# Performance work log

Hardware: AMD Instinct MI355X
Metric: run time of the kernel (lower is better)

The kernel has to match this reference:

```python
import jax, jax.numpy as jnp
import numpy as np

CORR_WIDTH = 48
H_RADIUS = 3
V_RADIUS = 3


def _unfold_patches(img, vr, hr):
    # img: [b, c, h, w] -> [b, c*(2vr+1)*(2hr+1), h, w], zero-padded 'same'
    # (equivalent to nn.Unfold with padding=(hr, vr); channel ordering differs
    # from torch but the SSD reduction sums over all patch channels, so the
    # result is identical.)
    return jax.lax.conv_general_dilated_patches(
        img,
        filter_shape=(2 * vr + 1, 2 * hr + 1),
        window_strides=(1, 1),
        padding=((vr, vr), (hr, hr)),
    )


def setup_inputs() -> dict:
    key = jax.random.key(0)
    k1, k2 = jax.random.split(key)
    im_left = jax.random.normal(k1, (2, 16, 128, 256), dtype=jnp.float32)
    im_right = jax.random.normal(k2, (2, 16, 128, 256), dtype=jnp.float32)
    return {"im_left": im_left, "im_right": im_right}


def reference(im_left, im_right):
    cw, hr, vr = CORR_WIDTH, H_RADIUS, V_RADIUS
    b, c, h, w = im_left.shape
    # pad left image on the right edge by cw-1 zeros (ZeroPad2d((0, cw-1, 0, 0)))
    ext_l = jnp.pad(im_left, ((0, 0), (0, 0), (0, 0), (0, cw - 1)))
    patches_l = _unfold_patches(ext_l, vr, hr)    # [b, C, h, w+cw-1]
    patches_r = _unfold_patches(im_right, vr, hr)  # [b, C, h, w]

    # For each disparity d: cost[:, :, :, d] = sum_C (patches_l[..., d:d+w] - patches_r)^2
    # scan over disparities keeps peak memory at O(b*C*h*w) instead of
    # materializing the full [b, C, h, w, cw] broadcast difference.
    def step(carry, d):
        sl = jax.lax.dynamic_slice_in_dim(patches_l, d, w, axis=3)  # [b,C,h,w]
        cost_d = jnp.sum(jnp.square(sl - patches_r), axis=1)        # [b,h,w]
        return carry, cost_d

    _, cost = jax.lax.scan(step, None, jnp.arange(cw))  # [cw, b, h, w]
    return jnp.transpose(cost, (1, 2, 3, 0))            # [b, h, w, cw]
```

## Files before the change

kernel.cpp:

```cpp
#include <hip/hip_runtime.h>
#include <stdint.h>

#define CW 48
#define HR 3
#define VR 3
#define BB 2
#define CC 16
#define HH 128
#define WW 256

#define LW 312
#define RW2 264
#define SW 264
#define FWD (WW*CW)
#define HSEG 8

__device__ __forceinline__ uint32_t bf16rn(float f) {
    uint32_t x = __builtin_bit_cast(uint32_t, f);
    uint32_t lsb = (x >> 16) & 1u;
    x += 0x7fffu + lsb;
    return x >> 16;
}

__global__ __launch_bounds__(512) void ssd_hraw(
    const float* __restrict__ Lg, const float* __restrict__ Rg,
    uint16_t* __restrict__ Hws)
{
    const int bid = blockIdx.x;
    const int y   = bid % HH;
    const int b   = bid / HH;
    const int tid = threadIdx.x;

    __shared__ float Lsh[CC * LW];
    __shared__ float Rsh[CC * RW2];
    __shared__ float Ssh[CW * SW];
    __shared__ float el[LW];
    __shared__ float er[RW2];

    for (int i = tid; i < CC * 56; i += 512) {
        int c = i / 56, j = i % 56;
        int idx = (j < 3) ? j : (256 + j);
        Lsh[c * LW + idx] = 0.f;
    }
    for (int i = tid; i < CC * 8; i += 512) {
        int c = i >> 3, j = i & 7;
        int idx = (j < 3) ? j : (256 + j);
        Rsh[c * RW2 + idx] = 0.f;
    }
    if (tid < 56) { int idx = (tid < 3) ? tid : (256 + tid); el[idx] = 0.f; }
    else if (tid < 64) { int j = tid - 56; int idx = (j < 3) ? j : (256 + j); er[idx] = 0.f; }

    {
        const int img = tid >> 8;
        const int col = tid & 255;
        const float* __restrict__ base =
            (img ? Rg : Lg) + ((size_t)b * CC) * (HH * WW) + (size_t)y * WW + col;
        float* sh = (img ? &Rsh[HR + col] : &Lsh[HR + col]);
        const int stride = img ? RW2 : LW;
        float e = 0.f;
        #pragma unroll
        for (int c = 0; c < CC; ++c) {
            float v = base[(size_t)c * (HH * WW)];
            sh[c * stride] = v;
            e = fmaf(v, v, e);
        }
        (img ? er : el)[HR + col] = e;
    }
    __syncthreads();

    const int chalf = tid >> 8;
    const int unit  = tid & 255;
    const int q     = unit >> 6;
    const int xi0   = (unit & 63) * 4;
    const int d0    = q * 12;

    float acc[12][4];
    #pragma unroll
    for (int dd = 0; dd < 12; ++dd)
        #pragma unroll
        for (int xv = 0; xv < 4; ++xv) acc[dd][xv] = 0.f;

    {
        const int c0 = chalf * 8;
        #pragma unroll
        for (int ci = 0; ci < 8; ++ci) {
            const int c = c0 + ci;
            const float4 rv = *(const float4*)&Rsh[c * RW2 + xi0];
            const float rr[4] = {rv.x, rv.y, rv.z, rv.w};
            float lv[16];
            #pragma unroll
            for (int k = 0; k < 4; ++k)
                *(float4*)&lv[4 * k] = *(const float4*)&Lsh[c * LW + xi0 + d0 + 4 * k];
            #pragma unroll
            for (int dd = 0; dd < 12; ++dd)
                #pragma unroll
                for (int xv = 0; xv < 4; ++xv)
                    acc[dd][xv] = fmaf(lv[dd + xv], rr[xv], acc[dd][xv]);
        }
    }

    if (chalf == 0) {
        float elv[16];
        #pragma unroll
        for (int k = 0; k < 4; ++k)
            *(float4*)&elv[4 * k] = *(const float4*)&el[xi0 + d0 + 4 * k];
        const float4 e4 = *(const float4*)&er[xi0];
        const float err4[4] = {e4.x, e4.y, e4.z, e4.w};
        #pragma unroll
        for (int dd = 0; dd < 12; ++dd) {
            float4 o;
            o.x = elv[dd + 0] + err4[0] - 2.f * acc[dd][0];
            o.y = elv[dd + 1] + err4[1] - 2.f * acc[dd][1];
            o.z = elv[dd + 2] + err4[2] - 2.f * acc[dd][2];
            o.w = elv[dd + 3] + err4[3] - 2.f * acc[dd][3];
            *(float4*)&Ssh[(d0 + dd) * SW + xi0] = o;
        }
    } else {
        for (int p = tid - 256; p < 6 * CW; p += 256) {
            int dd = p % CW;
            int xi = 256 + p / CW;
            float a = 0.f;
            #pragma unroll
            for (int c = 0; c < CC; ++c)
                a = fmaf(Lsh[c * LW + xi + dd], Rsh[c * RW2 + xi], a);
            Ssh[dd * SW + xi] = el[xi + dd] + er[xi] - 2.f * a;
        }
    }
    __syncthreads();

    if (chalf == 1) {
        #pragma unroll
        for (int dd = 0; dd < 12; ++dd) {
            float4 v = *(const float4*)&Ssh[(d0 + dd) * SW + xi0];
            v.x = fmaf(-2.f, acc[dd][0], v.x);
            v.y = fmaf(-2.f, acc[dd][1], v.y);
            v.z = fmaf(-2.f, acc[dd][2], v.z);
            v.w = fmaf(-2.f, acc[dd][3], v.w);
            *(float4*)&Ssh[(d0 + dd) * SW + xi0] = v;
        }
    }
    __syncthreads();

    {
        const int j   = tid & 127;
        const int qh  = tid >> 7;
        const int w0  = 2 * j;
        const int dh0 = qh * 12;
        float hs[12][2];
        #pragma unroll
        for (int dd = 0; dd < 12; ++dd) {
            const float* row = &Ssh[(dh0 + dd) * SW + w0];
            const float2 r0 = *(const float2*)&row[0];
            const float2 r1 = *(const float2*)&row[2];
            const float2 r2 = *(const float2*)&row[4];
            const float2 r3 = *(const float2*)&row[6];
            float h0 = r0.x + r0.y + r1.x + r1.y + r2.x + r2.y + r3.x;
            hs[dd][0] = h0;
            hs[dd][1] = h0 - r0.x + r3.y;
        }
        uint16_t* H = Hws + (size_t)(b * HH + y) * FWD;
        #pragma unroll
        for (int xv = 0; xv < 2; ++xv) {
            uint32_t pk[6];
            #pragma unroll
            for (int i = 0; i < 6; ++i)
                pk[i] = bf16rn(hs[2 * i][xv]) | (bf16rn(hs[2 * i + 1][xv]) << 16);
            uint32_t* p = (uint32_t*)(H + (size_t)(w0 + xv) * CW + dh0);
            *(uint2*)&p[0] = make_uint2(pk[0], pk[1]);
            *(uint2*)&p[2] = make_uint2(pk[2], pk[3]);
            *(uint2*)&p[4] = make_uint2(pk[4], pk[5]);
        }
    }
}

__global__ __launch_bounds__(256) void vbox(
    const uint16_t* __restrict__ Hws, float* __restrict__ out)
{
    const int bid = blockIdx.x;
    const int g   = bid % 24;
    const int hs  = (bid / 24) % (HH / HSEG);
    const int b   = bid / (24 * (HH / HSEG));
    const int f2  = g * 256 + threadIdx.x;
    const int h0  = hs * HSEG;

    const uint16_t* H = Hws + (size_t)b * HH * FWD + 2 * f2;
    float*          O = out + (size_t)b * HH * FWD + 2 * f2;

    float vlo[HSEG + 6], vhi[HSEG + 6];
    if (h0 >= 3 && h0 + HSEG + 2 < HH) {
        #pragma unroll
        for (int k = 0; k < HSEG + 6; ++k) {
            uint32_t u = *(const uint32_t*)&H[(size_t)(h0 - 3 + k) * FWD];
            vlo[k] = __builtin_bit_cast(float, u << 16);
            vhi[k] = __builtin_bit_cast(float, u & 0xffff0000u);
        }
    } else {
        #pragma unroll
        for (int k = 0; k < HSEG + 6; ++k) {
            int yy = h0 - 3 + k;
            if (yy >= 0 && yy < HH) {
                uint32_t u = *(const uint32_t*)&H[(size_t)yy * FWD];
                vlo[k] = __builtin_bit_cast(float, u << 16);
                vhi[k] = __builtin_bit_cast(float, u & 0xffff0000u);
            } else { vlo[k] = 0.f; vhi[k] = 0.f; }
        }
    }
    #pragma unroll
    for (int hi = 0; hi < HSEG; ++hi) {
        float slo = vlo[hi], shi = vhi[hi];
        #pragma unroll
        for (int k = 1; k < 7; ++k) { slo += vlo[hi + k]; shi += vhi[hi + k]; }
        *(float2*)&O[(size_t)(h0 + hi) * FWD] = make_float2(slo, shi);
    }
}

extern "C" void kernel_launch(void* const* d_in, const int* in_sizes, int n_in,
                              void* d_out, int out_size, void* d_ws, size_t ws_size,
                              hipStream_t stream) {
    const float* L = (const float*)d_in[0];
    const float* R = (const float*)d_in[1];
    float* outp = (float*)d_out;
    uint16_t* Hws = (uint16_t*)d_ws;

    ssd_hraw<<<dim3(BB * HH), 512, 0, stream>>>(L, R, Hws);
    vbox<<<dim3(BB * (HH / HSEG) * 24), 256, 0, stream>>>(Hws, outp);
}
```

Measured before the change: 21.40 us.

## Switch intermediate to fp16, vectorize row loads, use sliding-window vertical sums

Packs the horizontal box-sum intermediate as fp16 using hardware half2 conversion instead of manual bf16 rounding and shifting. The horizontal sum now reads each row with wider float4 loads. The vertical box filter uses a running sliding-window sum instead of recomputing seven-term sums per row. fp16 has a narrower range than bf16 and the sliding sum can accumulate rounding error, so accuracy could change. The float2 cv load is unused.

```diff
diff --git a/kernel.cpp b/kernel.cpp
--- a/kernel.cpp
+++ b/kernel.cpp
@@ -1,4 +1,5 @@
 #include <hip/hip_runtime.h>
+#include <hip/hip_fp16.h>
 #include <stdint.h>
 
 #define CW 48
@@ -15,11 +16,12 @@
 #define FWD (WW*CW)
 #define HSEG 8
 
-__device__ __forceinline__ uint32_t bf16rn(float f) {
-    uint32_t x = __builtin_bit_cast(uint32_t, f);
-    uint32_t lsb = (x >> 16) & 1u;
-    x += 0x7fffu + lsb;
-    return x >> 16;
+__device__ __forceinline__ uint32_t pkf16(float a, float b) {
+    __half2 h = __floats2half2_rn(a, b);
+    return __builtin_bit_cast(uint32_t, h);
+}
+__device__ __forceinline__ float2 upk16(uint32_t u) {
+    return __half22float2(__builtin_bit_cast(__half2, u));
 }
 
 __global__ __launch_bounds__(512) void ssd_hraw(
@@ -149,14 +151,13 @@
         float hs[12][2];
         #pragma unroll
         for (int dd = 0; dd < 12; ++dd) {
-            const float* row = &Ssh[(dh0 + dd) * SW + w0];
-            const float2 r0 = *(const float2*)&row[0];
-            const float2 r1 = *(const float2*)&row[2];
-            const float2 r2 = *(const float2*)&row[4];
-            const float2 r3 = *(const float2*)&row[6];
-            float h0 = r0.x + r0.y + r1.x + r1.y + r2.x + r2.y + r3.x;
+            const float* row = &Ssh[(dh0 + dd) * SW];
+            const float4 a  = *(const float4*)&row[w0];
+            const float4 bv = *(const float4*)&row[w0 + 4];
+            const float2 cv = *(const float2*)&row[w0 + 8];
+            float h0 = a.x + a.y + a.z + a.w + bv.x + bv.y + bv.z;
             hs[dd][0] = h0;
-            hs[dd][1] = h0 - r0.x + r3.y;
+            hs[dd][1] = h0 - a.x + bv.w;
         }
         uint16_t* H = Hws + (size_t)(b * HH + y) * FWD;
         #pragma unroll
@@ -164,7 +165,7 @@
             uint32_t pk[6];
             #pragma unroll
             for (int i = 0; i < 6; ++i)
-                pk[i] = bf16rn(hs[2 * i][xv]) | (bf16rn(hs[2 * i + 1][xv]) << 16);
+                pk[i] = pkf16(hs[2 * i][xv], hs[2 * i + 1][xv]);
             uint32_t* p = (uint32_t*)(H + (size_t)(w0 + xv) * CW + dh0);
             *(uint2*)&p[0] = make_uint2(pk[0], pk[1]);
             *(uint2*)&p[2] = make_uint2(pk[2], pk[3]);
@@ -190,26 +191,27 @@
     if (h0 >= 3 && h0 + HSEG + 2 < HH) {
         #pragma unroll
         for (int k = 0; k < HSEG + 6; ++k) {
-            uint32_t u = *(const uint32_t*)&H[(size_t)(h0 - 3 + k) * FWD];
-            vlo[k] = __builtin_bit_cast(float, u << 16);
-            vhi[k] = __builtin_bit_cast(float, u & 0xffff0000u);
+            float2 f = upk16(*(const uint32_t*)&H[(size_t)(h0 - 3 + k) * FWD]);
+            vlo[k] = f.x; vhi[k] = f.y;
         }
     } else {
         #pragma unroll
         for (int k = 0; k < HSEG + 6; ++k) {
             int yy = h0 - 3 + k;
             if (yy >= 0 && yy < HH) {
-                uint32_t u = *(const uint32_t*)&H[(size_t)yy * FWD];
-                vlo[k] = __builtin_bit_cast(float, u << 16);
-                vhi[k] = __builtin_bit_cast(float, u & 0xffff0000u);
+                float2 f = upk16(*(const uint32_t*)&H[(size_t)yy * FWD]);
+                vlo[k] = f.x; vhi[k] = f.y;
             } else { vlo[k] = 0.f; vhi[k] = 0.f; }
         }
     }
+
+    float slo = vlo[0] + vlo[1] + vlo[2] + vlo[3] + vlo[4] + vlo[5] + vlo[6];
+    float shi = vhi[0] + vhi[1] + vhi[2] + vhi[3] + vhi[4] + vhi[5] + vhi[6];
+    *(float2*)&O[(size_t)h0 * FWD] = make_float2(slo, shi);
     #pragma unroll
-    for (int hi = 0; hi < HSEG; ++hi) {
-        float slo = vlo[hi], shi = vhi[hi];
-        #pragma unroll
-        for (int k = 1; k < 7; ++k) { slo += vlo[hi + k]; shi += vhi[hi + k]; }
+    for (int hi = 1; hi < HSEG; ++hi) {
+        slo += vlo[hi + 6] - vlo[hi - 1];
+        shi += vhi[hi + 6] - vhi[hi - 1];
         *(float2*)&O[(size_t)(h0 + hi) * FWD] = make_float2(slo, shi);
     }
 }
```

Result: slower. 25.16 us (+17.6%).
